# Kernel optimization log

Hardware: AMD Instinct MI355X
Metric: run time of the kernel (lower is better)

Reference implementation:

```python
import jax, jax.numpy as jnp
import numpy as np
import math

B, T, C = 4, 2048, 1024
H, D = 16, 64            # num_heads, head_dim
ORIG_LEN = 4096
MIN_FREQ, MAX_FREQ = 0.5, 40.0


def setup_inputs() -> dict:
    key = jax.random.key(0)
    ks = jax.random.split(key, 6)
    x = jax.random.normal(ks[0], (B, T, C), dtype=jnp.float32)
    keep_idx = jnp.sort(jax.random.randint(ks[1], (B, T, 1), 0, ORIG_LEN), axis=1)
    W_qkv = jax.random.normal(ks[2], (C, 3 * C), dtype=jnp.float32) * (1.0 / math.sqrt(C))
    b_qkv = jnp.zeros((3 * C,), dtype=jnp.float32)
    W_proj = jax.random.normal(ks[3], (C, C), dtype=jnp.float32) * (1.0 / math.sqrt(C))
    b_proj = jnp.zeros((C,), dtype=jnp.float32)
    return {"x": x, "keep_idx": keep_idx, "original_seq_len": ORIG_LEN,
            "W_qkv": W_qkv, "b_qkv": b_qkv, "W_proj": W_proj, "b_proj": b_proj}


def _rope_angles(positions, orig_len):
    # positions: [b, t] float token positions in the ORIGINAL sequence.
    # golden_gate 1-D RoPE: normalized positions times geometric frequency band.
    half = D // 2
    freqs = MIN_FREQ * (MAX_FREQ / MIN_FREQ) ** (jnp.arange(half, dtype=jnp.float32) / (half - 1))
    pos_norm = positions / jnp.float32(orig_len)          # [b, t]
    return 2.0 * jnp.pi * pos_norm[:, :, None] * freqs    # [b, t, half]


def _apply_rope(x, cos, sin):
    # x: [b, h, t, d]; cos/sin: [b, 1, t, d/2]; rotate (first half, second half) pairs
    half = D // 2
    x1, x2 = x[..., :half], x[..., half:]
    return jnp.concatenate([x1 * cos - x2 * sin, x1 * sin + x2 * cos], axis=-1)


def reference(x, keep_idx, original_seq_len, W_qkv, b_qkv, W_proj, b_proj):
    b, t, c = x.shape
    # fused QKV projection + head split: (b,t,3c) -> (b,t,3,h,d) -> (b,h,t,3,d)
    qkv = (x @ W_qkv + b_qkv).reshape(b, t, 3, H, D).transpose(0, 3, 1, 2, 4)
    q, k, v = qkv[:, :, :, 0], qkv[:, :, :, 1], qkv[:, :, :, 2]  # each [b,h,t,d]

    positions = keep_idx[..., 0].astype(jnp.float32)             # [b, t]
    ang = _rope_angles(positions, original_seq_len)              # [b, t, d/2]
    cos = jnp.cos(ang)[:, None]                                  # [b,1,t,d/2]
    sin = jnp.sin(ang)[:, None]
    q = _apply_rope(q, cos, sin)
    k = _apply_rope(k, cos, sin)

    # dense non-causal scaled dot-product attention
    scale = 1.0 / math.sqrt(D)
    scores = jnp.einsum('bhqd,bhkd->bhqk', q, k) * scale
    attn = jax.nn.softmax(scores, axis=-1)
    out = jnp.einsum('bhqk,bhkd->bhqd', attn, v)                 # [b,h,t,d]

    out = out.transpose(0, 2, 1, 3).reshape(b, t, H * D)         # [b,t,c]
    return out @ W_proj + b_proj
```

## Files before the change

### kernel.cpp

```cpp
#include <hip/hip_runtime.h>
#include <hip/hip_bf16.h>
#include <math.h>

#define B_ 4
#define T_ 2048
#define C_ 1024
#define H_ 16
#define D_ 64

typedef __attribute__((ext_vector_type(8))) short bf16x8_t;
typedef __attribute__((ext_vector_type(4))) float f32x4_t;
typedef __attribute__((ext_vector_type(2))) unsigned int uiv2_t;

#define SHIFT2 32.0f

#define GLOAD_LDS16(gp, lp)                                                          \
    __builtin_amdgcn_global_load_lds(                                                \
        (const __attribute__((address_space(1))) void*)(gp),                         \
        (__attribute__((address_space(3))) void*)(lp), 16, 0, 0)

#define WAVE_ORDER() __builtin_amdgcn_wave_barrier()

__device__ inline short bf16bits(float f) {
    __hip_bfloat16 h = __float2bfloat16(f);
    return *reinterpret_cast<short*>(&h);
}

__device__ inline unsigned int pack2bf(float a, float b) {
    __hip_bfloat162 h = __float22bfloat162_rn(make_float2(a, b));
    return *reinterpret_cast<unsigned int*>(&h);
}

__global__ void xconv_kernel(const float* __restrict__ in,
                             __hip_bfloat16* __restrict__ out, int n4) {
    int i = blockIdx.x * blockDim.x + threadIdx.x;
    if (i < n4) {
        float4 v = *(const float4*)(in + (size_t)i * 4);
        uint2 u;
        u.x = pack2bf(v.x, v.y);
        u.y = pack2bf(v.z, v.w);
        *(uint2*)(out + (size_t)i * 4) = u;
    }
}

__global__ void rope_tab_kernel(const int* __restrict__ keep,
                                const int* __restrict__ orig,
                                float* __restrict__ tab) {
    int i = blockIdx.x * blockDim.x + threadIdx.x;
    int tok = i >> 5, d = i & 31;
    float freq = 0.5f * exp2f((float)d * (6.321928094887362f / 31.0f));
    float ang  = 6.283185307179586f * ((float)keep[tok] / (float)(*orig)) * freq;
    tab[(size_t)tok * 64 + d]      = cosf(ang);
    tab[(size_t)tok * 64 + 32 + d] = sinf(ang);
}

__global__ void transpose_conv_kernel(const float* __restrict__ in,
                                      __hip_bfloat16* __restrict__ out,
                                      int K, int N) {
    __shared__ float s[32][33];
    const int n0 = blockIdx.x * 32;
    const int k0 = blockIdx.y * 32;
    const int tx = threadIdx.x;
    const int ty = threadIdx.y;
#pragma unroll
    for (int yy = 0; yy < 32; yy += 8)
        s[ty + yy][tx] = in[(size_t)(k0 + ty + yy) * N + n0 + tx];
    __syncthreads();
#pragma unroll
    for (int yy = 0; yy < 32; yy += 8)
        out[(size_t)(n0 + ty + yy) * K + k0 + tx] = __float2bfloat16(s[tx][ty + yy]);
}

#define GTILE (128 * 32)

template <int MODE>
__global__ __launch_bounds__(256)
void gemm_kernel(const __hip_bfloat16* __restrict__ A,
                 const __hip_bfloat16* __restrict__ BT,
                 const float* __restrict__ bias,
                 float* __restrict__ out,
                 __hip_bfloat16* __restrict__ qbuf,
                 __hip_bfloat16* __restrict__ kbuf,
                 __hip_bfloat16* __restrict__ vtbuf,
                 const float* __restrict__ ropetab,
                 int M, int N, int K) {
    __shared__ __align__(16) __hip_bfloat16 GS[6 * GTILE];

    const int tid  = threadIdx.x;
    const int lane = tid & 63;
    const int wave = tid >> 6;
    const int wm   = wave >> 1;
    const int wn   = wave & 1;
    const int l15  = lane & 15;
    const int quad = lane >> 4;

    const int nT  = N >> 7;
    const int grp = blockIdx.x / (8 * nT);
    const int rem = blockIdx.x - grp * 8 * nT;
    const int m0  = (grp * 8 + (rem & 7)) * 128;
    const int n0  = (rem >> 3) * 128;

    f32x4_t acc[4][4];
#pragma unroll
    for (int i = 0; i < 4; i++)
#pragma unroll
        for (int j = 0; j < 4; j++) acc[i][j] = (f32x4_t)0.0f;

    const int lrow = lane >> 2;
    const int scol = ((lane & 3) ^ ((lane >> 4) & 3)) * 8;
    const __hip_bfloat16* gA  = A  + (size_t)(m0 + wave * 16 + lrow) * K + scol;
    const __hip_bfloat16* gA2 = gA + (size_t)64 * K;
    const __hip_bfloat16* gB  = BT + (size_t)(n0 + wave * 16 + lrow) * K + scol;
    const __hip_bfloat16* gB2 = gB + (size_t)64 * K;
    const int ldsW = wave * 16 * 32;

    const int NK = K >> 5;
    GLOAD_LDS16(gA,  GS + ldsW);
    GLOAD_LDS16(gA2, GS + ldsW + 64 * 32);
    GLOAD_LDS16(gB,  GS + 3 * GTILE + ldsW);
    GLOAD_LDS16(gB2, GS + 3 * GTILE + ldsW + 64 * 32);
    if (NK > 1) {
        GLOAD_LDS16(gA  + 32, GS + GTILE + ldsW);
        GLOAD_LDS16(gA2 + 32, GS + GTILE + ldsW + 64 * 32);
        GLOAD_LDS16(gB  + 32, GS + 3 * GTILE + GTILE + ldsW);
        GLOAD_LDS16(gB2 + 32, GS + 3 * GTILE + GTILE + ldsW + 64 * 32);
    }

    int off = 0;
    for (int t = 0; t < NK; ++t) {
        if (t + 2 < NK) {
            int poff = off + 2 * GTILE;
            if (poff >= 3 * GTILE) poff -= 3 * GTILE;
            const int kk = (t + 2) << 5;
            GLOAD_LDS16(gA  + kk, GS + poff + ldsW);
            GLOAD_LDS16(gA2 + kk, GS + poff + ldsW + 64 * 32);
            GLOAD_LDS16(gB  + kk, GS + 3 * GTILE + poff + ldsW);
            GLOAD_LDS16(gB2 + kk, GS + 3 * GTILE + poff + ldsW + 64 * 32);
            asm volatile("s_waitcnt vmcnt(8)" ::: "memory");
        } else if (t + 1 < NK) {
            asm volatile("s_waitcnt vmcnt(4)" ::: "memory");
        } else {
            asm volatile("s_waitcnt vmcnt(0)" ::: "memory");
        }
        __builtin_amdgcn_s_barrier();
        __builtin_amdgcn_sched_barrier(0);

        bf16x8_t af[4], bfv[4];
#pragma unroll
        for (int i = 0; i < 4; i++)
            af[i] = *(const bf16x8_t*)(GS + off + (wm * 64 + i * 16 + l15) * 32 +
                                       ((quad ^ (l15 >> 2)) * 8));
#pragma unroll
        for (int j = 0; j < 4; j++)
            bfv[j] = *(const bf16x8_t*)(GS + 3 * GTILE + off + (wn * 64 + j * 16 + l15) * 32 +
                                        ((quad ^ (l15 >> 2)) * 8));
#pragma unroll
        for (int i = 0; i < 4; i++)
#pragma unroll
            for (int j = 0; j < 4; j++)
                acc[i][j] = __builtin_amdgcn_mfma_f32_16x16x32_bf16(af[i], bfv[j], acc[i][j], 0, 0, 0);

        __builtin_amdgcn_sched_barrier(0);
        asm volatile("s_waitcnt lgkmcnt(0)" ::: "memory");
        __builtin_amdgcn_s_barrier();

        off += GTILE;
        if (off == 3 * GTILE) off = 0;
    }

    float bv[4];
#pragma unroll
    for (int j = 0; j < 4; j++)
        bv[j] = bias[n0 + wn * 64 + j * 16 + l15];

    if (MODE == 0) {
#pragma unroll
        for (int i = 0; i < 4; i++)
#pragma unroll
            for (int r = 0; r < 4; r++) {
                int row = m0 + wm * 64 + i * 16 + quad * 4 + r;
#pragma unroll
                for (int j = 0; j < 4; j++) {
                    int col = n0 + wn * 64 + j * 16 + l15;
                    out[(size_t)row * N + col] = acc[i][j][r] + bv[j];
                }
            }
    } else {
        const int cb   = n0 + wn * 64;
        const int part = cb >> 10;
        if (part == 2) {
            const int hb = (n0 & 1023) >> 6;
            __hip_bfloat16* myL = GS + wn * (64 * 136);
#pragma unroll
            for (int j = 0; j < 4; j++)
#pragma unroll
                for (int i = 0; i < 4; i++)
#pragma unroll
                    for (int r = 0; r < 4; r++) {
                        int rt = wm * 64 + i * 16 + quad * 4 + r;
                        int d  = j * 16 + l15;
                        myL[d * 136 + rt] = __float2bfloat16(acc[i][j][r] + bv[j]);
                    }
            __syncthreads();
            const int bb  = m0 >> 11;
            const int t0  = m0 & 2047;
            const int row = tid >> 1;
            const int wn2 = row >> 6;
            const int dd  = row & 63;
            const __hip_bfloat16* src = GS + wn2 * (64 * 136) + dd * 136;
            __hip_bfloat16* dstv = vtbuf +
                ((size_t)((bb * H_ + hb + wn2) * D_ + dd)) * T_ + t0;
#pragma unroll
            for (int s = 0; s < 8; s++) {
                int ch = (tid & 1) * 8 + s;
                *(bf16x8_t*)(dstv + ch * 8) = *(const bf16x8_t*)(src + ch * 8);
            }
        } else {
            const int h = (cb & 1023) >> 6;
            __hip_bfloat16* dst = (part == 0) ? qbuf : kbuf;
            const float sc = (part == 0) ? 0.18033688011112042f : 1.0f;
#pragma unroll
            for (int i = 0; i < 4; i++) {
#pragma unroll
                for (int r = 0; r < 4; r++) {
                    int row = m0 + wm * 64 + i * 16 + quad * 4 + r;
                    int b = row >> 11;
                    int t = row & 2047;
                    const float* trow = ropetab + (size_t)row * 64;
                    size_t base = ((size_t)(b * H_ + h) * T_ + t) * D_;
#pragma unroll
                    for (int j = 0; j < 2; j++) {
                        int d = j * 16 + l15;
                        float cs = trow[d];
                        float sn = trow[32 + d];
                        float x1 = acc[i][j][r]     + bv[j];
                        float x2 = acc[i][j + 2][r] + bv[j + 2];
                        dst[base + d]      = __float2bfloat16(sc * (x1 * cs - x2 * sn));
                        dst[base + d + 32] = __float2bfloat16(sc * (x1 * sn + x2 * cs));
                    }
                }
            }
        }
    }
}

#define KVTILE (64 * 64)

__global__ __launch_bounds__(256, 4)
void attn_kernel(const __hip_bfloat16* __restrict__ q,
                 const __hip_bfloat16* __restrict__ k,
                 const __hip_bfloat16* __restrict__ vt,
                 __hip_bfloat16* __restrict__ attn_out) {
    __shared__ __align__(16) __hip_bfloat16 SMEM[4 * KVTILE];

    const int tid  = threadIdx.x;
    const int lane = tid & 63;
    const int wave = tid >> 6;
    const int l15  = lane & 15;
    const int quad = lane >> 4;
    const int x7   = l15 & 7;

    const int bh = blockIdx.x & 63;
    const int qt = blockIdx.x >> 6;
    const int b  = bh >> 4;
    const int h  = bh & 15;

    const size_t qkbase = (size_t)bh * T_ * D_;
    const size_t vbase  = (size_t)bh * D_ * T_;
    const int    qrow0  = qt * 128 + wave * 32;

    const int drow   = lane >> 3;
    const int gchunk = (lane & 7) ^ drow;

    const __hip_bfloat16* kg = k + qkbase;
    const __hip_bfloat16* vg = vt + vbase;

    const int c0 = ((quad)     ^ x7) * 8;
    const int c1 = ((4 + quad) ^ x7) * 8;

    bf16x8_t qa[2][2];
#pragma unroll
    for (int qf = 0; qf < 2; qf++)
#pragma unroll
        for (int kk = 0; kk < 2; kk++)
            qa[qf][kk] = *(const bf16x8_t*)(q + qkbase +
                          (size_t)(qrow0 + qf * 16 + l15) * D_ + kk * 32 + quad * 8);

    bf16x8_t ones;
#pragma unroll
    for (int i = 0; i < 8; i++) ones[i] = (short)0x3F80;

    const f32x4_t mbias = (f32x4_t)(-SHIFT2);

    f32x4_t o[2][4];
#pragma unroll
    for (int qf = 0; qf < 2; qf++)
#pragma unroll
        for (int jd = 0; jd < 4; jd++) o[qf][jd] = (f32x4_t)0.0f;
    f32x4_t osum[2];
    osum[0] = (f32x4_t)0.0f;
    osum[1] = (f32x4_t)0.0f;

#pragma unroll
    for (int i = 0; i < 2; i++) {
        int r = wave * 16 + i * 8;
        GLOAD_LDS16(kg + (size_t)(r + drow) * D_ + gchunk * 8, SMEM + r * 64);
        GLOAD_LDS16(vg + (size_t)(r + drow) * T_ + gchunk * 8, SMEM + 2 * KVTILE + r * 64);
    }

    for (int kt = 0; kt < T_ / 64; kt++) {
        const int curoff = (kt & 1) * KVTILE;
        const int nxtoff = curoff ^ KVTILE;
        if (kt + 1 < T_ / 64) {
#pragma unroll
            for (int i = 0; i < 2; i++) {
                int r = wave * 16 + i * 8;
                GLOAD_LDS16(kg + (size_t)((kt + 1) * 64 + r + drow) * D_ + gchunk * 8,
                            SMEM + nxtoff + r * 64);
                GLOAD_LDS16(vg + (size_t)(r + drow) * T_ + (kt + 1) * 64 + gchunk * 8,
                            SMEM + 2 * KVTILE + nxtoff + r * 64);
            }
            asm volatile("s_waitcnt vmcnt(4)" ::: "memory");
        } else {
            asm volatile("s_waitcnt vmcnt(0)" ::: "memory");
        }
        __builtin_amdgcn_s_barrier();
        __builtin_amdgcn_sched_barrier(0);

        const __hip_bfloat16* KLc = SMEM + curoff;
        const __hip_bfloat16* VLc = SMEM + 2 * KVTILE + curoff;

        bf16x8_t kf[4][2];
#pragma unroll
        for (int jt = 0; jt < 4; jt++) {
            kf[jt][0] = *(const bf16x8_t*)(KLc + (jt * 16 + l15) * 64 + c0);
            kf[jt][1] = *(const bf16x8_t*)(KLc + (jt * 16 + l15) * 64 + c1);
        }

        f32x4_t sT[2][4];
        __builtin_amdgcn_s_setprio(1);
#pragma unroll
        for (int jt = 0; jt < 4; jt++)
#pragma unroll
            for (int qf = 0; qf < 2; qf++) {
                sT[qf][jt] = __builtin_amdgcn_mfma_f32_16x16x32_bf16(
                    kf[jt][0], qa[qf][0], mbias, 0, 0, 0);
                sT[qf][jt] = __builtin_amdgcn_mfma_f32_16x16x32_bf16(
                    kf[jt][1], qa[qf][1], sT[qf][jt], 0, 0, 0);
            }
        __builtin_amdgcn_s_setprio(0);

        bf16x8_t pb[2][2];
#pragma unroll
        for (int qf = 0; qf < 2; qf++) {
            unsigned int w0[4], w1[4];
#pragma unroll
            for (int jt = 0; jt < 4; jt++) {
                float p0 = __builtin_amdgcn_exp2f(sT[qf][jt][0]);
                float p1 = __builtin_amdgcn_exp2f(sT[qf][jt][1]);
                float p2 = __builtin_amdgcn_exp2f(sT[qf][jt][2]);
                float p3 = __builtin_amdgcn_exp2f(sT[qf][jt][3]);
                w0[jt] = pack2bf(p0, p1);
                w1[jt] = pack2bf(p2, p3);
            }
#pragma unroll
            for (int kk = 0; kk < 2; kk++) {
                uiv2_t s0 = __builtin_amdgcn_permlane32_swap(w0[2 * kk], w0[2 * kk + 1], false, false);
                uiv2_t r0 = __builtin_amdgcn_permlane16_swap(s0[0], s0[1], false, false);
                uiv2_t s1 = __builtin_amdgcn_permlane32_swap(w1[2 * kk], w1[2 * kk + 1], false, false);
                uiv2_t r1 = __builtin_amdgcn_permlane16_swap(s1[0], s1[1], false, false);
                union { unsigned int u[4]; bf16x8_t v; } pu;
                pu.u[0] = r0[0];
                pu.u[1] = r1[0];
                pu.u[2] = r0[1];
                pu.u[3] = r1[1];
                pb[qf][kk] = pu.v;
            }
        }

        __builtin_amdgcn_s_setprio(1);
#pragma unroll
        for (int qf = 0; qf < 2; qf++) {
            osum[qf] = __builtin_amdgcn_mfma_f32_16x16x32_bf16(ones, pb[qf][0], osum[qf], 0, 0, 0);
            osum[qf] = __builtin_amdgcn_mfma_f32_16x16x32_bf16(ones, pb[qf][1], osum[qf], 0, 0, 0);
        }

#pragma unroll
        for (int jd = 0; jd < 4; jd++) {
            bf16x8_t vf0 = *(const bf16x8_t*)(VLc + (jd * 16 + l15) * 64 + c0);
            bf16x8_t vf1 = *(const bf16x8_t*)(VLc + (jd * 16 + l15) * 64 + c1);
#pragma unroll
            for (int qf = 0; qf < 2; qf++) {
                o[qf][jd] = __builtin_amdgcn_mfma_f32_16x16x32_bf16(vf0, pb[qf][0], o[qf][jd], 0, 0, 0);
                o[qf][jd] = __builtin_amdgcn_mfma_f32_16x16x32_bf16(vf1, pb[qf][1], o[qf][jd], 0, 0, 0);
            }
        }
        __builtin_amdgcn_s_setprio(0);

        __builtin_amdgcn_sched_barrier(0);
        asm volatile("s_waitcnt lgkmcnt(0)" ::: "memory");
        __builtin_amdgcn_s_barrier();
    }

    float inv[2];
    inv[0] = 1.0f / osum[0][0];
    inv[1] = 1.0f / osum[1][0];

    __hip_bfloat16* Pep = SMEM + wave * (32 * 72);

    WAVE_ORDER();
#pragma unroll
    for (int qf = 0; qf < 2; qf++) {
#pragma unroll
        for (int jd = 0; jd < 4; jd++) {
            uint2 pk;
            pk.x = pack2bf(o[qf][jd][0] * inv[qf], o[qf][jd][1] * inv[qf]);
            pk.y = pack2bf(o[qf][jd][2] * inv[qf], o[qf][jd][3] * inv[qf]);
            *(uint2*)(Pep + (qf * 16 + l15) * 72 + jd * 16 + quad * 4) = pk;
        }
    }
    WAVE_ORDER();

#pragma unroll
    for (int rnd = 0; rnd < 4; rnd++) {
        int row = rnd * 8 + (lane >> 3);
        int col = (lane & 7) * 8;
        bf16x8_t vrow = *(const bf16x8_t*)(Pep + row * 72 + col);
        int token = qt * 128 + wave * 32 + row;
        *(bf16x8_t*)(attn_out + ((size_t)(b * T_ + token)) * C_ + h * 64 + col) = vrow;
    }
}

extern "C" void kernel_launch(void* const* d_in, const int* in_sizes, int n_in,
                              void* d_out, int out_size, void* d_ws, size_t ws_size,
                              hipStream_t stream) {
    const float* x        = (const float*)d_in[0];
    const int*   keep_idx = (const int*)d_in[1];
    const int*   orig_len = (const int*)d_in[2];
    const float* Wqkv     = (const float*)d_in[3];
    const float* bqkv     = (const float*)d_in[4];
    const float* Wproj    = (const float*)d_in[5];
    const float* bproj    = (const float*)d_in[6];
    float*       out      = (float*)d_out;

    const size_t NTOK = (size_t)B_ * T_;
    const size_t QKV1 = NTOK * C_;

    __hip_bfloat16* qbuf    = (__hip_bfloat16*)d_ws;
    __hip_bfloat16* kbuf    = qbuf    + QKV1;
    __hip_bfloat16* vtbuf   = kbuf    + QKV1;
    __hip_bfloat16* attnbuf = vtbuf   + QKV1;
    __hip_bfloat16* WqkvT   = attnbuf + QKV1;
    __hip_bfloat16* WprojT  = WqkvT   + (size_t)C_ * 3 * C_;
    __hip_bfloat16* xbf     = WprojT  + (size_t)C_ * C_;
    float*          ropetab = (float*)(xbf + QKV1);

    xconv_kernel<<<(QKV1 / 4 + 255) / 256, 256, 0, stream>>>(x, xbf, (int)(QKV1 / 4));
    rope_tab_kernel<<<(NTOK * 32) / 256, 256, 0, stream>>>(keep_idx, orig_len, ropetab);

    dim3 tb(32, 8);
    transpose_conv_kernel<<<dim3(3 * C_ / 32, C_ / 32), tb, 0, stream>>>(Wqkv, WqkvT, C_, 3 * C_);
    transpose_conv_kernel<<<dim3(C_ / 32, C_ / 32), tb, 0, stream>>>(Wproj, WprojT, C_, C_);

    gemm_kernel<1><<<(8192 / 128) * (3072 / 128), 256, 0, stream>>>(
        xbf, WqkvT, bqkv, nullptr, qbuf, kbuf, vtbuf, ropetab, 8192, 3072, 1024);

    attn_kernel<<<(T_ / 128) * 64, 256, 0, stream>>>(qbuf, kbuf, vtbuf, attnbuf);

    gemm_kernel<0><<<(8192 / 128) * (1024 / 128), 256, 0, stream>>>(
        attnbuf, WprojT, bproj, out, nullptr, nullptr, nullptr, nullptr, 8192, 1024, 1024);
}
```

Measured before the change: 269.9 us.

## Double attention query tile per block to 256 rows, 64 per wave

Each attention workgroup now handles 256 query rows instead of 128, with each wave owning 64 rows (4 query fragments). Every K/V tile loaded into LDS is therefore reused across twice as many queries, halving K/V global traffic and LDS fragment loads per unit of work. The S computation is interleaved per query fragment to limit live score registers. The grid halves to 512 blocks and occupancy drops to 2 blocks per CU because accumulator and Q registers double. That may reduce latency hiding and leave the GPU less filled.

New measurement: 270.8 us. No clear change (+0.4%).

```diff
diff --git a/kernel.cpp b/kernel.cpp
--- a/kernel.cpp
+++ b/kernel.cpp
@@ -246,7 +246,7 @@
 
 #define KVTILE (64 * 64)
 
-__global__ __launch_bounds__(256, 4)
+__global__ __launch_bounds__(256, 2)
 void attn_kernel(const __hip_bfloat16* __restrict__ q,
                  const __hip_bfloat16* __restrict__ k,
                  const __hip_bfloat16* __restrict__ vt,
@@ -267,7 +267,7 @@
 
     const size_t qkbase = (size_t)bh * T_ * D_;
     const size_t vbase  = (size_t)bh * D_ * T_;
-    const int    qrow0  = qt * 128 + wave * 32;
+    const int    qrow0  = qt * 256 + wave * 64;
 
     const int drow   = lane >> 3;
     const int gchunk = (lane & 7) ^ drow;
@@ -278,9 +278,9 @@
     const int c0 = ((quad)     ^ x7) * 8;
     const int c1 = ((4 + quad) ^ x7) * 8;
 
-    bf16x8_t qa[2][2];
-#pragma unroll
-    for (int qf = 0; qf < 2; qf++)
+    bf16x8_t qa[4][2];
+#pragma unroll
+    for (int qf = 0; qf < 4; qf++)
 #pragma unroll
         for (int kk = 0; kk < 2; kk++)
             qa[qf][kk] = *(const bf16x8_t*)(q + qkbase +
@@ -292,14 +292,14 @@
 
     const f32x4_t mbias = (f32x4_t)(-SHIFT2);
 
-    f32x4_t o[2][4];
-#pragma unroll
-    for (int qf = 0; qf < 2; qf++)
+    f32x4_t o[4][4];
+#pragma unroll
+    for (int qf = 0; qf < 4; qf++)
 #pragma unroll
         for (int jd = 0; jd < 4; jd++) o[qf][jd] = (f32x4_t)0.0f;
-    f32x4_t osum[2];
-    osum[0] = (f32x4_t)0.0f;
-    osum[1] = (f32x4_t)0.0f;
+    f32x4_t osum[4];
+#pragma unroll
+    for (int qf = 0; qf < 4; qf++) osum[qf] = (f32x4_t)0.0f;
 
 #pragma unroll
     for (int i = 0; i < 2; i++) {
@@ -337,29 +337,27 @@
             kf[jt][1] = *(const bf16x8_t*)(KLc + (jt * 16 + l15) * 64 + c1);
         }
 
-        f32x4_t sT[2][4];
-        __builtin_amdgcn_s_setprio(1);
-#pragma unroll
-        for (int jt = 0; jt < 4; jt++)
-#pragma unroll
-            for (int qf = 0; qf < 2; qf++) {
-                sT[qf][jt] = __builtin_amdgcn_mfma_f32_16x16x32_bf16(
+        bf16x8_t pb[4][2];
+#pragma unroll
+        for (int qf = 0; qf < 4; qf++) {
+            f32x4_t sT[4];
+            __builtin_amdgcn_s_setprio(1);
+#pragma unroll
+            for (int jt = 0; jt < 4; jt++) {
+                sT[jt] = __builtin_amdgcn_mfma_f32_16x16x32_bf16(
                     kf[jt][0], qa[qf][0], mbias, 0, 0, 0);
-                sT[qf][jt] = __builtin_amdgcn_mfma_f32_16x16x32_bf16(
-                    kf[jt][1], qa[qf][1], sT[qf][jt], 0, 0, 0);
-            }
-        __builtin_amdgcn_s_setprio(0);
-
-        bf16x8_t pb[2][2];
-#pragma unroll
-        for (int qf = 0; qf < 2; qf++) {
+                sT[jt] = __builtin_amdgcn_mfma_f32_16x16x32_bf16(
+                    kf[jt][1], qa[qf][1], sT[jt], 0, 0, 0);
+            }
+            __builtin_amdgcn_s_setprio(0);
+
             unsigned int w0[4], w1[4];
 #pragma unroll
             for (int jt = 0; jt < 4; jt++) {
-                float p0 = __builtin_amdgcn_exp2f(sT[qf][jt][0]);
-                float p1 = __builtin_amdgcn_exp2f(sT[qf][jt][1]);
-                float p2 = __builtin_amdgcn_exp2f(sT[qf][jt][2]);
-                float p3 = __builtin_amdgcn_exp2f(sT[qf][jt][3]);
+                float p0 = __builtin_amdgcn_exp2f(sT[jt][0]);
+                float p1 = __builtin_amdgcn_exp2f(sT[jt][1]);
+                float p2 = __builtin_amdgcn_exp2f(sT[jt][2]);
+                float p3 = __builtin_amdgcn_exp2f(sT[jt][3]);
                 w0[jt] = pack2bf(p0, p1);
                 w1[jt] = pack2bf(p2, p3);
             }
@@ -380,7 +378,7 @@
 
         __builtin_amdgcn_s_setprio(1);
 #pragma unroll
-        for (int qf = 0; qf < 2; qf++) {
+        for (int qf = 0; qf < 4; qf++) {
             osum[qf] = __builtin_amdgcn_mfma_f32_16x16x32_bf16(ones, pb[qf][0], osum[qf], 0, 0, 0);
             osum[qf] = __builtin_amdgcn_mfma_f32_16x16x32_bf16(ones, pb[qf][1], osum[qf], 0, 0, 0);
         }
@@ -390,7 +388,7 @@
             bf16x8_t vf0 = *(const bf16x8_t*)(VLc + (jd * 16 + l15) * 64 + c0);
             bf16x8_t vf1 = *(const bf16x8_t*)(VLc + (jd * 16 + l15) * 64 + c1);
 #pragma unroll
-            for (int qf = 0; qf < 2; qf++) {
+            for (int qf = 0; qf < 4; qf++) {
                 o[qf][jd] = __builtin_amdgcn_mfma_f32_16x16x32_bf16(vf0, pb[qf][0], o[qf][jd], 0, 0, 0);
                 o[qf][jd] = __builtin_amdgcn_mfma_f32_16x16x32_bf16(vf1, pb[qf][1], o[qf][jd], 0, 0, 0);
             }
@@ -402,32 +400,35 @@
         __builtin_amdgcn_s_barrier();
     }
 
-    float inv[2];
-    inv[0] = 1.0f / osum[0][0];
-    inv[1] = 1.0f / osum[1][0];
+    float inv[4];
+#pragma unroll
+    for (int qf = 0; qf < 4; qf++) inv[qf] = 1.0f / osum[qf][0];
 
     __hip_bfloat16* Pep = SMEM + wave * (32 * 72);
 
-    WAVE_ORDER();
-#pragma unroll
-    for (int qf = 0; qf < 2; qf++) {
-#pragma unroll
-        for (int jd = 0; jd < 4; jd++) {
-            uint2 pk;
-            pk.x = pack2bf(o[qf][jd][0] * inv[qf], o[qf][jd][1] * inv[qf]);
-            pk.y = pack2bf(o[qf][jd][2] * inv[qf], o[qf][jd][3] * inv[qf]);
-            *(uint2*)(Pep + (qf * 16 + l15) * 72 + jd * 16 + quad * 4) = pk;
-        }
-    }
-    WAVE_ORDER();
-
-#pragma unroll
-    for (int rnd = 0; rnd < 4; rnd++) {
-        int row = rnd * 8 + (lane >> 3);
-        int col = (lane & 7) * 8;
-        bf16x8_t vrow = *(const bf16x8_t*)(Pep + row * 72 + col);
-        int token = qt * 128 + wave * 32 + row;
-        *(bf16x8_t*)(attn_out + ((size_t)(b * T_ + token)) * C_ + h * 64 + col) = vrow;
+#pragma unroll
+    for (int p = 0; p < 2; p++) {
+        WAVE_ORDER();
+#pragma unroll
+        for (int qh = 0; qh < 2; qh++) {
+            int qf = p * 2 + qh;
+#pragma unroll
+            for (int jd = 0; jd < 4; jd++) {
+                uint2 pk;
+                pk.x = pack2bf(o[qf][jd][0] * inv[qf], o[qf][jd][1] * inv[qf]);
+                pk.y = pack2bf(o[qf][jd][2] * inv[qf], o[qf][jd][3] * inv[qf]);
+                *(uint2*)(Pep + (qh * 16 + l15) * 72 + jd * 16 + quad * 4) = pk;
+            }
+        }
+        WAVE_ORDER();
+#pragma unroll
+        for (int rnd = 0; rnd < 4; rnd++) {
+            int row = rnd * 8 + (lane >> 3);
+            int col = (lane & 7) * 8;
+            bf16x8_t vrow = *(const bf16x8_t*)(Pep + row * 72 + col);
+            int token = qt * 256 + wave * 64 + p * 32 + row;
+            *(bf16x8_t*)(attn_out + ((size_t)(b * T_ + token)) * C_ + h * 64 + col) = vrow;
+        }
     }
 }
 
@@ -465,7 +466,7 @@
     gemm_kernel<1><<<(8192 / 128) * (3072 / 128), 256, 0, stream>>>(
         xbf, WqkvT, bqkv, nullptr, qbuf, kbuf, vtbuf, ropetab, 8192, 3072, 1024);
 
-    attn_kernel<<<(T_ / 128) * 64, 256, 0, stream>>>(qbuf, kbuf, vtbuf, attnbuf);
+    attn_kernel<<<(T_ / 256) * 64, 256, 0, stream>>>(qbuf, kbuf, vtbuf, attnbuf);
 
     gemm_kernel<0><<<(8192 / 128) * (1024 / 128), 256, 0, stream>>>(
         attnbuf, WprojT, bproj, out, nullptr, nullptr, nullptr, nullptr, 8192, 1024, 1024);
```
